# Kernel optimization log

Measured on AMD Instinct MI355X. Metric: run time of the kernel, lower is better.

Reference implementation:

```python
import jax, jax.numpy as jnp
import numpy as np

ALPHA = 0.05   # propalpha
GDEP = 2       # gcn_depth
DIL = 2        # new_dilation
KSET = (2, 3, 6, 7)

def _dconv(x, w, b, d):
    # Conv2d(c_in, c_out, (1, k), dilation=(1, d), padding='same'), NCHW layout
    k = w.shape[-1]
    tot = d * (k - 1)
    lo = tot // 2
    y = jax.lax.conv_general_dilated(x, w, (1, 1), ((0, 0), (lo, tot - lo)),
                                     rhs_dilation=(1, d),
                                     dimension_numbers=('NCHW', 'OIHW', 'NCHW'))
    return y + b[None, :, None, None]

def _inception(x, ws, bs):
    # 'same' padding keeps seq_len for every branch, so the tail-slice is a no-op
    return jnp.concatenate([_dconv(x, w, b, DIL) for w, b in zip(ws, bs)], axis=1)

def _gcn(Hf, Aoff, W, b, n):
    # PyG GCNConv with unit edge weights (no edge_weight passed) and remaining self-loops:
    # out = D^-1/2 (A_off + I_R)^T D^-1/2 (Hf @ W^T) + b, where only rows < n carry edges.
    XW = Hf @ W.T
    deg = jnp.ones((Hf.shape[0],), Hf.dtype).at[:n].add(jnp.sum(Aoff, axis=0))
    dis = jax.lax.rsqrt(deg)
    out = XW / deg[:, None]                                           # self-loop term
    out = out.at[:n].add(dis[:n, None] * (Aoff.T @ (dis[:n, None] * XW[:n])))
    return out + b[None, :]

def _mixprop(X, A, gws, gbs, mw, mb):
    B, C, n, L = X.shape
    # dense_to_sparse ignores weights here (none passed to GCNConv) -> binary adjacency;
    # add_remaining_self_loops replaces any diagonal entries, so zero the diagonal.
    Aoff = (A != 0).astype(X.dtype) * (1.0 - jnp.eye(n, dtype=X.dtype))
    H = X
    hops = [X]
    for i in range(GDEP):
        Hf = H.reshape(B * L, C * n)   # torch row-major reshape, replicated exactly
        H1 = _gcn(Hf, Aoff, gws[i], gbs[i], n)
        H = ALPHA * X + H1.reshape(B, C, n, L)
        hops.append(H)
    Hc = jnp.concatenate(hops, axis=1)  # (B, (GDEP+1)*C, n, L)
    return jnp.einsum('bixl,oi->boxl', Hc, mw) + mb[None, :, None, None]

def _layernorm(x, w, b, idx, eps=1e-5):
    # F.layer_norm over all of x.shape[1:] with node-indexed affine params
    mu = jnp.mean(x, axis=(1, 2, 3), keepdims=True)
    var = jnp.var(x, axis=(1, 2, 3), keepdims=True)
    xh = (x - mu) * jax.lax.rsqrt(var + eps)
    return xh * w[:, idx, :][None] + b[:, idx, :][None]

def _forward(x, x_skip, A, idx, fws, fbs, gws, gbs, skip_w, skip_b,
             mp1_gw, mp1_gb, mp1_mw, mp1_mb, mp2_gw, mp2_gb, mp2_mw, mp2_mb,
             ln_w, ln_b):
    x_res = x
    xf = jnp.tanh(_inception(x, fws, fbs))
    xg = jax.nn.sigmoid(_inception(x, gws, gbs))
    x = xf * xg  # gated dilated temporal conv (dropout is an eval-mode no-op)
    x_skip = jnp.einsum('bixl,oi->boxl', x, skip_w) + skip_b[None, :, None, None] + x_skip
    x = (_mixprop(x, A, mp1_gw, mp1_gb, mp1_mw, mp1_mb)
         + _mixprop(x.swapaxes(0, 0), A.T, mp2_gw, mp2_gb, mp2_mw, mp2_mb))
    x = x + x_res[..., -x.shape[3]:]
    x = _layernorm(x, ln_w, ln_b, idx)
    return x, x_skip

def setup_inputs():
    key = jax.random.key(0)
    ks = jax.random.split(key, 32)
    B, C, N, L, SKIP = 16, 32, 128, 128, 64
    F = C * N
    co = C // len(KSET)
    d = {}
    d['x'] = jax.random.normal(ks[0], (B, C, N, L), jnp.float32)
    d['x_skip'] = jax.random.normal(ks[1], (B, SKIP, N, L), jnp.float32)
    d['A'] = jax.random.uniform(ks[2], (N, N), jnp.float32)
    d['idx'] = jnp.arange(N, dtype=jnp.int32)
    i = 3
    for pre in ('f', 'g'):
        for k in KSET:
            d[pre + 'w' + str(k)] = jax.random.normal(ks[i], (co, C, 1, k), jnp.float32) * float(1.0 / np.sqrt(C * k))
            d[pre + 'b' + str(k)] = jax.random.uniform(ks[i + 1], (co,), jnp.float32)
            i += 2
    d['skip_w'] = jax.random.normal(ks[i], (SKIP, C), jnp.float32) * float(1.0 / np.sqrt(C)); i += 1
    d['skip_b'] = jax.random.uniform(ks[i], (SKIP,), jnp.float32); i += 1
    for mp in ('mp1', 'mp2'):
        d[mp + '_gw'] = jax.random.normal(ks[i], (GDEP, F, F), jnp.float32) * float(1.0 / np.sqrt(F)); i += 1
        d[mp + '_gb'] = jnp.zeros((GDEP, F), jnp.float32)
        d[mp + '_mw'] = jax.random.normal(ks[i], (C, (GDEP + 1) * C), jnp.float32) * float(1.0 / np.sqrt((GDEP + 1) * C)); i += 1
        d[mp + '_mb'] = jax.random.uniform(ks[i], (C,), jnp.float32); i += 1
    d['ln_w'] = jnp.ones((C, N, L), jnp.float32)
    d['ln_b'] = jnp.zeros((C, N, L), jnp.float32)
    return d

def reference(x, x_skip, A, idx, fw2, fb2, fw3, fb3, fw6, fb6, fw7, fb7,
              gw2, gb2, gw3, gb3, gw6, gb6, gw7, gb7, skip_w, skip_b,
              mp1_gw, mp1_gb, mp1_mw, mp1_mb, mp2_gw, mp2_gb, mp2_mw, mp2_mb,
              ln_w, ln_b):
    return _forward(x, x_skip, A, idx,
                    [fw2, fw3, fw6, fw7], [fb2, fb3, fb6, fb7],
                    [gw2, gw3, gw6, gw7], [gb2, gb3, gb6, gb7],
                    skip_w, skip_b, mp1_gw, mp1_gb, mp1_mw, mp1_mb,
                    mp2_gw, mp2_gb, mp2_mw, mp2_mb, ln_w, ln_b)
```

## Files before the change

### kernel.cpp

```cpp
#include <hip/hip_runtime.h>
#include <stdint.h>

typedef unsigned short u16;
typedef unsigned int   u32;
typedef __attribute__((ext_vector_type(4))) float f32x4;
typedef __attribute__((ext_vector_type(8))) short bf16x8;

__device__ __forceinline__ u16 f2bf(float f) {
    u32 i = __float_as_uint(f);
    u32 r = (i + 0x7fffu + ((i >> 16) & 1u)) >> 16;
    return (u16)r;
}
__device__ __forceinline__ float bf2f(u16 u) {
    return __uint_as_float(((u32)u) << 16);
}
__device__ __forceinline__ u32 cvt2bf(float a, float b) {
    u32 r;
    asm("v_cvt_pk_bf16_f32 %0, %1, %2" : "=v"(r) : "v"(a), "v"(b));
    return r;
}

#define GLOAD16(g, l) __builtin_amdgcn_global_load_lds( \
    (const __attribute__((address_space(1))) void*)(g), \
    (__attribute__((address_space(3))) void*)(l), 16, 0, 0)

#define RAW_BARRIER()  asm volatile("s_barrier" ::: "memory")
#define VMCNT(n)       asm volatile("s_waitcnt vmcnt(" #n ")" ::: "memory")

__global__ void k_prep(const float* __restrict__ A, float* dis1, float* inv1,
                       float* dis2, float* inv2)
{
    int r = threadIdx.x;
    if (r >= 128) return;
    int cc = 0, cr = 0;
    for (int j = 0; j < 128; ++j) {
        if (j == r) continue;
        if (A[(j << 7) + r] != 0.f) cc++;
        if (A[(r << 7) + j] != 0.f) cr++;
    }
    float d1 = 1.f + (float)cc, d2 = 1.f + (float)cr;
    dis1[r] = rsqrtf(d1); inv1[r] = 1.f / d1;
    dis2[r] = rsqrtf(d2); inv2[r] = 1.f / d2;
}

__global__ __launch_bounds__(256)
void k_wcvt2(const float* __restrict__ W0, const float* __restrict__ W1,
             u16* __restrict__ Wb0, u16* __restrict__ Wb1)
{
    int half = blockIdx.x >> 13;
    const float* W = half ? W1 : W0;
    u16* Wb = half ? Wb1 : Wb0;
    size_t e = ((size_t)(blockIdx.x & 8191) * 256 + threadIdx.x) * 8;
    f32x4 a = *(const f32x4*)(W + e);
    f32x4 b = *(const f32x4*)(W + e + 4);
    uint4 r;
    r.x = cvt2bf(a[0], a[1]); r.y = cvt2bf(a[2], a[3]);
    r.z = cvt2bf(b[0], b[1]); r.w = cvt2bf(b[2], b[3]);
    *(uint4*)(Wb + e) = r;
}

__global__ __launch_bounds__(512, 1)
void k_gemm2g(const u16* __restrict__ A0, const u16* __restrict__ A1,
              const u16* __restrict__ B0, const u16* __restrict__ B1,
              const u16* __restrict__ Gres,
              const float* __restrict__ gb0, const float* __restrict__ gb1,
              u16* __restrict__ Ha, u16* __restrict__ Hb,
              float* __restrict__ XW0a, float* __restrict__ XW0b)
{
    __shared__ alignas(16) u16 LDS[65536];
    const int NT = 128;
    const int tid  = threadIdx.x;
    const int lane = tid & 63;
    const int wid  = tid >> 6;
    const int wr = wid >> 2, wc = wid & 3;

    const int bid = blockIdx.x;
    const int swz = (bid & 7) * 32 + (bid >> 3);
    const int z   = swz >> 7;
    const int rem = swz & 127;
    const int bm = (rem >> 4) * 256;
    const int bn = (rem & 15) * 256;

    const u16* Ap = (z ? A1 : A0) + (size_t)bm * 4096;
    const u16* Bp = (z ? B1 : B0) + (size_t)bn * 4096;

    int aoff[8], boff[4];
    #pragma unroll
    for (int i = 0; i < 8; ++i) {
        int row = wr * 128 + i * 16 + (lane & 15);
        int sp  = (lane >> 4) ^ ((row >> 1) & 3);
        aoff[i] = row * 32 + sp * 8;
    }
    #pragma unroll
    for (int j = 0; j < 4; ++j) {
        int row = wc * 64 + j * 16 + (lane & 15);
        int sp  = (lane >> 4) ^ ((row >> 1) & 3);
        boff[j] = row * 32 + sp * 8;
    }

    auto stage = [&](int t) {
        const int k0  = t << 5;
        u16* buf = LDS + ((t & 3) << 14);
        #pragma unroll
        for (int h = 0; h < 2; ++h) {
            const int c  = tid + h * 512;
            const int r  = c >> 2;
            const int sl = (c & 3) ^ ((r >> 1) & 3);
            GLOAD16(Ap + (size_t)r * 4096 + k0 + sl * 8, buf + c * 8);
            GLOAD16(Bp + (size_t)r * 4096 + k0 + sl * 8, buf + 8192 + c * 8);
        }
    };

    f32x4 acc[8][4] = {};

    auto compute = [&](int t) {
        const u16* buf = LDS + ((t & 3) << 14);
        bf16x8 af[8], bf[4];
        #pragma unroll
        for (int j = 0; j < 4; ++j) bf[j] = *(const bf16x8*)(buf + 8192 + boff[j]);
        #pragma unroll
        for (int i = 0; i < 8; ++i) af[i] = *(const bf16x8*)(buf + aoff[i]);
        __builtin_amdgcn_s_setprio(1);
        #pragma unroll
        for (int i = 0; i < 8; ++i)
            #pragma unroll
            for (int j = 0; j < 4; ++j)
                acc[i][j] = __builtin_amdgcn_mfma_f32_16x16x32_bf16(af[i], bf[j], acc[i][j], 0, 0, 0);
        __builtin_amdgcn_s_setprio(0);
    };

    stage(0); stage(1); stage(2);
    for (int t = 0; t < NT - 3; ++t) {
        VMCNT(8);
        RAW_BARRIER();
        stage(t + 3);
        compute(t);
    }
    VMCNT(8);  RAW_BARRIER(); compute(NT - 3);
    VMCNT(4);  RAW_BARRIER(); compute(NT - 2);
    VMCNT(0);  RAW_BARRIER(); compute(NT - 1);

    const int orow = (lane >> 4) * 4, ocol = lane & 15;
    const float* gbv = z ? gb1 : gb0;
    u16* H = z ? Hb : Ha;

    #pragma unroll
    for (int j = 0; j < 4; ++j) {
        const int o = bn + wc * 64 + j * 16 + ocol;
        const float gbo = gbv[o];
        #pragma unroll
        for (int i = 0; i < 8; ++i) {
            const int rbase = bm + wr * 128 + i * 16 + orow;
            #pragma unroll
            for (int v = 0; v < 4; ++v) {
                const size_t e = (size_t)(rbase + v) * 4096 + o;
                float g = bf2f(Gres[e]);
                H[e] = f2bf(__fmaf_rn(0.05f, g, acc[i][j][v] + gbo));
            }
        }
    }
    if (bm == 0 && wr == 0) {
        float* XW0 = z ? XW0b : XW0a;
        #pragma unroll
        for (int i = 0; i < 8; ++i) {
            #pragma unroll
            for (int j = 0; j < 4; ++j) {
                float* cp = XW0 + (size_t)(i * 16 + orow) * 4096 + (bn + wc * 64 + j * 16 + ocol);
                #pragma unroll
                for (int v = 0; v < 4; ++v)
                    cp[(size_t)v * 4096] = acc[i][j][v];
            }
        }
    }
}

__global__ __launch_bounds__(256)
void k_gcnfix(const float* __restrict__ XW0a, const float* __restrict__ XW0b,
              const u16* __restrict__ G, const float* __restrict__ Af,
              const float* __restrict__ dis1, const float* __restrict__ inv1,
              const float* __restrict__ dis2, const float* __restrict__ inv2,
              const float* __restrict__ gb0, const float* __restrict__ gb1,
              u16* __restrict__ Ha, u16* __restrict__ Hb)
{
    const int prob = blockIdx.x >> 9;
    const int rem  = blockIdx.x & 511;
    const int t4 = rem * 256 + threadIdx.x;
    const int r = t4 >> 10, og = (t4 & 1023) << 2;
    const float* XW0 = prob ? XW0b : XW0a;
    const float* dis = prob ? dis2 : dis1;
    const float* inv = prob ? inv2 : inv1;
    const float* gb  = prob ? gb1  : gb0;
    u16* H = prob ? Hb : Ha;

    const size_t e = ((size_t)r << 12) + og;
    f32x4 xw = *(const f32x4*)(XW0 + e);
    f32x4 s = {0.f, 0.f, 0.f, 0.f};
    for (int j = 0; j < 128; ++j) {
        float av = prob ? Af[(r << 7) + j] : Af[(j << 7) + r];
        float wv = ((av != 0.f) && (j != r)) ? dis[j] : 0.f;
        f32x4 xv = *(const f32x4*)(XW0 + ((size_t)j << 12) + og);
        #pragma unroll
        for (int q = 0; q < 4; ++q) s[q] = __fmaf_rn(wv, xv[q], s[q]);
    }
    const float iv = inv[r], dr = dis[r];
    f32x4 gb4 = *(const f32x4*)(gb + og);
    uint2 gv = *(const uint2*)(G + e);
    float g0 = __uint_as_float(gv.x << 16), g1 = __uint_as_float(gv.x & 0xffff0000u);
    float g2 = __uint_as_float(gv.y << 16), g3 = __uint_as_float(gv.y & 0xffff0000u);
    float y0 = __fmaf_rn(0.05f, g0, __fmaf_rn(dr, s[0], xw[0] * iv) + gb4[0]);
    float y1 = __fmaf_rn(0.05f, g1, __fmaf_rn(dr, s[1], xw[1] * iv) + gb4[1]);
    float y2 = __fmaf_rn(0.05f, g2, __fmaf_rn(dr, s[2], xw[2] * iv) + gb4[2]);
    float y3 = __fmaf_rn(0.05f, g3, __fmaf_rn(dr, s[3], xw[3] * iv) + gb4[3]);
    uint2 rr;
    rr.x = cvt2bf(y0, y1);
    rr.y = cvt2bf(y2, y3);
    *(uint2*)(H + e) = rr;
}

__device__ __forceinline__ constexpr int wbase_of(int k) {
    return k == 2 ? 0 : k == 3 ? 520 : k == 6 ? 1296 : 2840;
}
__device__ __forceinline__ constexpr int ob_of(int k) {
    return k == 2 ? 0 : k == 3 ? 8 : k == 6 ? 16 : 24;
}

template<int K_>
__device__ __forceinline__ void conv_phase(const float* __restrict__ xsb,
                                           const float* __restrict__ wfp,
                                           const float* __restrict__ wgp,
                                           float fb, float gb,
                                           u16* __restrict__ Gp)
{
    float accf[8], accg[8];
    #pragma unroll
    for (int i = 0; i < 8; ++i) { accf[i] = fb; accg[i] = gb; }
    for (int c = 0; c < 32; ++c) {
        float xw[24];
        const float* xr = xsb + c * 144;
        #pragma unroll
        for (int q = 0; q < 6; ++q) {
            f32x4 v = *(const f32x4*)(xr + q * 4);
            xw[q * 4 + 0] = v[0]; xw[q * 4 + 1] = v[1];
            xw[q * 4 + 2] = v[2]; xw[q * 4 + 3] = v[3];
        }
        float wfj[K_], wgj[K_];
        const float* wfc = wfp + c * K_;
        const float* wgc = wgp + c * K_;
        #pragma unroll
        for (int j = 0; j < K_; ++j) { wfj[j] = wfc[j]; wgj[j] = wgc[j]; }
        #pragma unroll
        for (int li = 0; li < 8; ++li) {
            #pragma unroll
            for (int j = 0; j < K_; ++j) {
                float xv = xw[li + 8 - (K_ - 1) + 2 * j];
                accf[li] = __fmaf_rn(xv, wfj[j], accf[li]);
                accg[li] = __fmaf_rn(xv, wgj[j], accg[li]);
            }
        }
    }
    u16 o8[8];
    #pragma unroll
    for (int i = 0; i < 8; ++i) {
        float e2 = __expf(2.f * accf[i]);
        float th = 1.f - __fdividef(2.f, e2 + 1.f);
        float sg = __fdividef(1.f, 1.f + __expf(-accg[i]));
        o8[i] = f2bf(th * sg);
    }
    uint4 u;
    u.x = o8[0] | ((u32)o8[1] << 16); u.y = o8[2] | ((u32)o8[3] << 16);
    u.z = o8[4] | ((u32)o8[5] << 16); u.w = o8[6] | ((u32)o8[7] << 16);
    *(uint4*)Gp = u;
}

template<int KA, int KB>
__device__ __forceinline__ void wave_pair(const float* __restrict__ xs,
                                          const float* __restrict__ wfl,
                                          const float* __restrict__ wgl,
                                          const float* __restrict__ fbl,
                                          const float* __restrict__ gbl,
                                          int oo, int lL, int b, int n,
                                          u16* __restrict__ G)
{
    {
        constexpr int BS = wbase_of(KA), ST = 32 * KA + 1, OB = ob_of(KA);
        const int o = OB + oo, l0 = lL * 8;
        conv_phase<KA>(xs + l0, wfl + BS + oo * ST, wgl + BS + oo * ST,
                       fbl[o], gbl[o],
                       G + (((size_t)(b * 32 + o) * 128 + n) * 128 + l0));
    }
    {
        constexpr int BS = wbase_of(KB), ST = 32 * KB + 1, OB = ob_of(KB);
        const int o = OB + oo, l0 = 64 + lL * 8;
        conv_phase<KB>(xs + l0, wfl + BS + oo * ST, wgl + BS + oo * ST,
                       fbl[o], gbl[o],
                       G + (((size_t)(b * 32 + o) * 128 + n) * 128 + l0));
    }
}

__global__ __launch_bounds__(256)
void k_incep(const float* __restrict__ x,
             const float* __restrict__ fw2p, const float* __restrict__ fw3p,
             const float* __restrict__ fw6p, const float* __restrict__ fw7p,
             const float* __restrict__ fb2p, const float* __restrict__ fb3p,
             const float* __restrict__ fb6p, const float* __restrict__ fb7p,
             const float* __restrict__ gw2p, const float* __restrict__ gw3p,
             const float* __restrict__ gw6p, const float* __restrict__ gw7p,
             const float* __restrict__ gb2p, const float* __restrict__ gb3p,
             const float* __restrict__ gb6p, const float* __restrict__ gb7p,
             u16* __restrict__ G)
{
    __shared__ alignas(16) float xs[32 * 144];
    __shared__ float wfl[4640], wgl[4640];
    __shared__ float fbl[32], gbl[32];
    const int tid = threadIdx.x;
    const int b = blockIdx.x >> 7, n = blockIdx.x & 127;

    for (int i = tid; i < 32 * 144; i += 256) xs[i] = 0.f;
    for (int g = tid; g < 4608; g += 256) {
        int rel, k, woff;
        const float *pf, *pg;
        if (g < 512)       { rel = g;        k = 2; woff = 0;    pf = fw2p; pg = gw2p; }
        else if (g < 1280) { rel = g - 512;  k = 3; woff = 520;  pf = fw3p; pg = gw3p; }
        else if (g < 2816) { rel = g - 1280; k = 6; woff = 1296; pf = fw6p; pg = gw6p; }
        else               { rel = g - 2816; k = 7; woff = 2840; pf = fw7p; pg = gw7p; }
        int ck = 32 * k;
        int oo = rel / ck, rem = rel % ck;
        int dst = woff + oo * (ck + 1) + rem;
        wfl[dst] = pf[rel];
        wgl[dst] = pg[rel];
    }
    if (tid < 32) {
        int br = tid >> 3, oo = tid & 7;
        const float* pf = br == 0 ? fb2p : br == 1 ? fb3p : br == 2 ? fb6p : fb7p;
        const float* pg = br == 0 ? gb2p : br == 1 ? gb3p : br == 2 ? gb6p : gb7p;
        fbl[tid] = pf[oo]; gbl[tid] = pg[oo];
    }
    __syncthreads();
    const float* xb = x + (size_t)b * 524288 + n * 128;
    for (int p = 0; p < 4; ++p) {
        int chunk = p * 256 + tid;
        int c = chunk >> 5, l4 = (chunk & 31) * 4;
        *(f32x4*)&xs[c * 144 + 8 + l4] = *(const f32x4*)(xb + (size_t)c * 16384 + l4);
    }
    __syncthreads();

    const int w = tid >> 6, lane = tid & 63;
    const int oo = lane >> 3, lL = lane & 7;
    switch (w) {
        case 0:  wave_pair<2, 7>(xs, wfl, wgl, fbl, gbl, oo, lL, b, n, G); break;
        case 1:  wave_pair<7, 2>(xs, wfl, wgl, fbl, gbl, oo, lL, b, n, G); break;
        case 2:  wave_pair<3, 6>(xs, wfl, wgl, fbl, gbl, oo, lL, b, n, G); break;
        default: wave_pair<6, 3>(xs, wfl, wgl, fbl, gbl, oo, lL, b, n, G); break;
    }
}

__global__ __launch_bounds__(256)
void k_skip(const u16* __restrict__ G, const float* __restrict__ xskip,
            const float* __restrict__ sw, const float* __restrict__ sb,
            float* __restrict__ outp)
{
    __shared__ alignas(16) u16 Gs[4096];
    __shared__ float swl[64 * 33];
    __shared__ float sbl[64];
    const int tid = threadIdx.x;
    const int b = blockIdx.x >> 7, n = blockIdx.x & 127;
    const u16* gb_ = G + (size_t)b * 524288 + n * 128;
    for (int p = 0; p < 2; ++p) {
        int chunk = p * 256 + tid, c = chunk >> 4, l8 = (chunk & 15) * 8;
        *(uint4*)&Gs[c * 128 + l8] = *(const uint4*)(gb_ + (size_t)c * 16384 + l8);
    }
    for (int i = tid; i < 2048; i += 256) swl[(i >> 5) * 33 + (i & 31)] = sw[i];
    if (tid < 64) sbl[tid] = sb[tid];
    __syncthreads();
    const int sg = (tid & 15) * 4, l0 = (tid >> 4) * 8;
    float acc[4][8];
    #pragma unroll
    for (int si = 0; si < 4; ++si) {
        float bv = sbl[sg + si];
        #pragma unroll
        for (int li = 0; li < 8; ++li) acc[si][li] = bv;
    }
    for (int c = 0; c < 32; ++c) {
        uint4 gv = *(const uint4*)&Gs[c * 128 + l0];
        float g[8];
        g[0] = __uint_as_float(gv.x << 16); g[1] = __uint_as_float(gv.x & 0xffff0000u);
        g[2] = __uint_as_float(gv.y << 16); g[3] = __uint_as_float(gv.y & 0xffff0000u);
        g[4] = __uint_as_float(gv.z << 16); g[5] = __uint_as_float(gv.z & 0xffff0000u);
        g[6] = __uint_as_float(gv.w << 16); g[7] = __uint_as_float(gv.w & 0xffff0000u);
        #pragma unroll
        for (int si = 0; si < 4; ++si) {
            float wv = swl[(sg + si) * 33 + c];
            #pragma unroll
            for (int li = 0; li < 8; ++li) acc[si][li] = __fmaf_rn(g[li], wv, acc[si][li]);
        }
    }
    #pragma unroll
    for (int si = 0; si < 4; ++si) {
        size_t e = ((size_t)(b * 64 + sg + si) * 128 + n) * 128 + l0;
        f32x4 x0 = *(const f32x4*)(xskip + e);
        f32x4 x1 = *(const f32x4*)(xskip + e + 4);
        f32x4 r0, r1;
        r0[0] = acc[si][0] + x0[0]; r0[1] = acc[si][1] + x0[1];
        r0[2] = acc[si][2] + x0[2]; r0[3] = acc[si][3] + x0[3];
        r1[0] = acc[si][4] + x1[0]; r1[1] = acc[si][5] + x1[1];
        r1[2] = acc[si][6] + x1[2]; r1[3] = acc[si][7] + x1[3];
        *(f32x4*)(outp + e)     = r0;
        *(f32x4*)(outp + e + 4) = r1;
    }
}

__global__ __launch_bounds__(256)
void k_mix2ln(const u16* __restrict__ G,
              const u16* __restrict__ H1, const u16* __restrict__ H2,
              const u16* __restrict__ H1b, const u16* __restrict__ H2b,
              const float* __restrict__ mw1, const float* __restrict__ mb1,
              const float* __restrict__ mw2, const float* __restrict__ mb2,
              const float* __restrict__ x,
              float* __restrict__ Y, float* __restrict__ partial)
{
    __shared__ alignas(16) u16 Gs[4096], H1s[4096], H2s[4096], H1bs[4096], H2bs[4096];
    __shared__ float wSg[32 * 33], wS11[32 * 33], wS12[32 * 33], wS21[32 * 33], wS22[32 * 33];
    __shared__ float mbl[32];
    const int tid = threadIdx.x;
    const int b = blockIdx.x >> 7, xn = blockIdx.x & 127;
    size_t base = (size_t)b * 524288 + xn * 128;
    for (int p = 0; p < 2; ++p) {
        int chunk = p * 256 + tid, c = chunk >> 4, l8 = (chunk & 15) * 8;
        size_t src = base + (size_t)c * 16384 + l8;
        *(uint4*)&Gs[c * 128 + l8]   = *(const uint4*)(G + src);
        *(uint4*)&H1s[c * 128 + l8]  = *(const uint4*)(H1 + src);
        *(uint4*)&H2s[c * 128 + l8]  = *(const uint4*)(H2 + src);
        *(uint4*)&H1bs[c * 128 + l8] = *(const uint4*)(H1b + src);
        *(uint4*)&H2bs[c * 128 + l8] = *(const uint4*)(H2b + src);
    }
    for (int i = tid; i < 1024; i += 256) {
        int o = i >> 5, c = i & 31;
        int d = o * 33 + c;
        wSg[d]  = mw1[o * 96 + c] + mw2[o * 96 + c];
        wS11[d] = mw1[o * 96 + 32 + c];
        wS12[d] = mw1[o * 96 + 64 + c];
        wS21[d] = mw2[o * 96 + 32 + c];
        wS22[d] = mw2[o * 96 + 64 + c];
    }
    if (tid < 32) mbl[tid] = mb1[tid] + mb2[tid];
    __syncthreads();
    const int og = (tid & 7) * 4, l0 = (tid >> 3) * 4;
    float acc[4][4];
    #pragma unroll
    for (int oi = 0; oi < 4; ++oi) {
        float bv = mbl[og + oi];
        acc[oi][0] = bv; acc[oi][1] = bv; acc[oi][2] = bv; acc[oi][3] = bv;
    }
    for (int c = 0; c < 32; ++c) {
        uint2 ga = *(const uint2*)&Gs[c * 128 + l0];
        uint2 h1 = *(const uint2*)&H1s[c * 128 + l0];
        uint2 h2 = *(const uint2*)&H2s[c * 128 + l0];
        uint2 j1 = *(const uint2*)&H1bs[c * 128 + l0];
        uint2 j2 = *(const uint2*)&H2bs[c * 128 + l0];
        float gv[4], v1[4], v2[4], u1[4], u2[4];
        gv[0] = __uint_as_float(ga.x << 16); gv[1] = __uint_as_float(ga.x & 0xffff0000u);
        gv[2] = __uint_as_float(ga.y << 16); gv[3] = __uint_as_float(ga.y & 0xffff0000u);
        v1[0] = __uint_as_float(h1.x << 16); v1[1] = __uint_as_float(h1.x & 0xffff0000u);
        v1[2] = __uint_as_float(h1.y << 16); v1[3] = __uint_as_float(h1.y & 0xffff0000u);
        v2[0] = __uint_as_float(h2.x << 16); v2[1] = __uint_as_float(h2.x & 0xffff0000u);
        v2[2] = __uint_as_float(h2.y << 16); v2[3] = __uint_as_float(h2.y & 0xffff0000u);
        u1[0] = __uint_as_float(j1.x << 16); u1[1] = __uint_as_float(j1.x & 0xffff0000u);
        u1[2] = __uint_as_float(j1.y << 16); u1[3] = __uint_as_float(j1.y & 0xffff0000u);
        u2[0] = __uint_as_float(j2.x << 16); u2[1] = __uint_as_float(j2.x & 0xffff0000u);
        u2[2] = __uint_as_float(j2.y << 16); u2[3] = __uint_as_float(j2.y & 0xffff0000u);
        #pragma unroll
        for (int oi = 0; oi < 4; ++oi) {
            int d = (og + oi) * 33 + c;
            float a0 = wSg[d], a1 = wS11[d], a2 = wS12[d], a3 = wS21[d], a4 = wS22[d];
            #pragma unroll
            for (int li = 0; li < 4; ++li)
                acc[oi][li] += gv[li] * a0 + v1[li] * a1 + v2[li] * a2
                             + u1[li] * a3 + u2[li] * a4;
        }
    }
    float s = 0.f, ss = 0.f;
    #pragma unroll
    for (int oi = 0; oi < 4; ++oi) {
        size_t e = ((size_t)(b * 32 + og + oi) * 128 + xn) * 128 + l0;
        f32x4 xv = *(const f32x4*)(x + e);
        f32x4 yv;
        #pragma unroll
        for (int li = 0; li < 4; ++li) {
            float y = acc[oi][li] + xv[li];
            yv[li] = y;
            s += y; ss += y * y;
        }
        *(f32x4*)(Y + e) = yv;
    }
    #pragma unroll
    for (int o = 32; o > 0; o >>= 1) {
        s  += __shfl_down(s,  o, 64);
        ss += __shfl_down(ss, o, 64);
    }
    __shared__ float sred[8];
    int w = tid >> 6;
    if ((tid & 63) == 0) { sred[w * 2] = s; sred[w * 2 + 1] = ss; }
    __syncthreads();
    if (tid == 0) {
        partial[blockIdx.x * 2]     = sred[0] + sred[2] + sred[4] + sred[6];
        partial[blockIdx.x * 2 + 1] = sred[1] + sred[3] + sred[5] + sred[7];
    }
}

__global__ __launch_bounds__(256)
void k_lnnorm(const float* __restrict__ Y,
              const float* __restrict__ partial, const int* __restrict__ idxp,
              const float* __restrict__ lnw, const float* __restrict__ lnb,
              float* __restrict__ outx)
{
    const int tid = threadIdx.x;
    const int b = blockIdx.x >> 7, chunk = blockIdx.x & 127;
    float s = 0.f, ss = 0.f;
    if (tid < 128) {
        s  = partial[(b * 128 + tid) * 2];
        ss = partial[(b * 128 + tid) * 2 + 1];
    }
    #pragma unroll
    for (int o = 32; o > 0; o >>= 1) {
        s  += __shfl_down(s,  o, 64);
        ss += __shfl_down(ss, o, 64);
    }
    __shared__ float sred[4];
    __shared__ float mv[2];
    if ((tid & 63) == 0 && tid < 128) { sred[(tid >> 6) * 2] = s; sred[(tid >> 6) * 2 + 1] = ss; }
    __syncthreads();
    if (tid == 0) {
        float S = sred[0] + sred[2], SS = sred[1] + sred[3];
        float mean = S * (1.f / 524288.f);
        float var = SS * (1.f / 524288.f) - mean * mean;
        mv[0] = mean; mv[1] = rsqrtf(var + 1e-5f);
    }
    __syncthreads();
    const float mean = mv[0], rstd = mv[1];
    #pragma unroll
    for (int q = 0; q < 4; ++q) {
        int ib = chunk * 4096 + q * 1024 + tid * 4;
        size_t e = (size_t)b * 524288 + ib;
        f32x4 yv = *(const f32x4*)(Y + e);
        int c = ib >> 14, xn = (ib >> 7) & 127, l = ib & 127;
        int ix = idxp[xn];
        size_t we = ((size_t)c * 128 + ix) * 128 + l;
        f32x4 wv = *(const f32x4*)(lnw + we);
        f32x4 bv = *(const f32x4*)(lnb + we);
        f32x4 r;
        #pragma unroll
        for (int j = 0; j < 4; ++j)
            r[j] = (yv[j] - mean) * rstd * wv[j] + bv[j];
        *(f32x4*)(outx + e) = r;
    }
}

extern "C" void kernel_launch(void* const* d_in, const int* in_sizes, int n_in,
                              void* d_out, int out_size, void* d_ws, size_t ws_size,
                              hipStream_t stream)
{
    (void)in_sizes; (void)n_in; (void)out_size; (void)ws_size;
    const float* x      = (const float*)d_in[0];
    const float* xskip  = (const float*)d_in[1];
    const float* A      = (const float*)d_in[2];
    const int*   idxp   = (const int*)d_in[3];
    const float* fw2p = (const float*)d_in[4];  const float* fb2p = (const float*)d_in[5];
    const float* fw3p = (const float*)d_in[6];  const float* fb3p = (const float*)d_in[7];
    const float* fw6p = (const float*)d_in[8];  const float* fb6p = (const float*)d_in[9];
    const float* fw7p = (const float*)d_in[10]; const float* fb7p = (const float*)d_in[11];
    const float* gw2p = (const float*)d_in[12]; const float* gb2p = (const float*)d_in[13];
    const float* gw3p = (const float*)d_in[14]; const float* gb3p = (const float*)d_in[15];
    const float* gw6p = (const float*)d_in[16]; const float* gb6p = (const float*)d_in[17];
    const float* gw7p = (const float*)d_in[18]; const float* gb7p = (const float*)d_in[19];
    const float* sw   = (const float*)d_in[20]; const float* sb   = (const float*)d_in[21];
    const float* mp1_gw = (const float*)d_in[22]; const float* mp1_gb = (const float*)d_in[23];
    const float* mp1_mw = (const float*)d_in[24]; const float* mp1_mb = (const float*)d_in[25];
    const float* mp2_gw = (const float*)d_in[26]; const float* mp2_gb = (const float*)d_in[27];
    const float* mp2_mw = (const float*)d_in[28]; const float* mp2_mb = (const float*)d_in[29];
    const float* lnw = (const float*)d_in[30]; const float* lnb = (const float*)d_in[31];

    char* wsb = (char*)d_ws;
    float* out_x  = (float*)d_out;
    float* out_sk = out_x + 8388608;

    const size_t MB16 = 16777216, MB33 = 33554432;
    u16*   G    = (u16*)(wsb);
    u16*   H1   = (u16*)(wsb + MB16);
    u16*   H1b  = (u16*)(wsb + 2 * MB16);
    u16*   H2   = (u16*)(wsb + 3 * MB16);
    u16*   H2b  = (u16*)(wsb + 4 * MB16);
    u16*   Wb0  = (u16*)(wsb + 5 * MB16);
    u16*   Wb1  = (u16*)(wsb + 5 * MB16 + MB33);
    float* Yb   = (float*)Wb0;
    float* XW0a = (float*)(wsb + 5 * MB16 + 2 * MB33);
    float* XW0b = (float*)(wsb + 5 * MB16 + 2 * MB33 + 2097152);
    float* part = (float*)(wsb + 5 * MB16 + 2 * MB33 + 4194304);
    float* dd   = (float*)(wsb + 5 * MB16 + 2 * MB33 + 4194304 + 16384);
    float *dis1 = dd, *inv1 = dd + 128, *dis2 = dd + 256, *inv2 = dd + 384;

    k_prep<<<1, 128, 0, stream>>>(A, dis1, inv1, dis2, inv2);
    k_incep<<<2048, 256, 0, stream>>>(x, fw2p, fw3p, fw6p, fw7p, fb2p, fb3p, fb6p, fb7p,
                                      gw2p, gw3p, gw6p, gw7p, gb2p, gb3p, gb6p, gb7p, G);
    k_skip<<<2048, 256, 0, stream>>>(G, xskip, sw, sb, out_sk);

    k_wcvt2<<<16384, 256, 0, stream>>>(mp1_gw, mp2_gw, Wb0, Wb1);
    k_gemm2g<<<256, 512, 0, stream>>>(G, G, Wb0, Wb1, G, mp1_gb, mp2_gb,
                                      H1, H1b, XW0a, XW0b);
    k_gcnfix<<<1024, 256, 0, stream>>>(XW0a, XW0b, G, A, dis1, inv1, dis2, inv2,
                                       mp1_gb, mp2_gb, H1, H1b);
    k_wcvt2<<<16384, 256, 0, stream>>>(mp1_gw + MB16, mp2_gw + MB16, Wb0, Wb1);
    k_gemm2g<<<256, 512, 0, stream>>>(H1, H1b, Wb0, Wb1, G, mp1_gb + 4096, mp2_gb + 4096,
                                      H2, H2b, XW0a, XW0b);
    k_gcnfix<<<1024, 256, 0, stream>>>(XW0a, XW0b, G, A, dis1, inv1, dis2, inv2,
                                       mp1_gb + 4096, mp2_gb + 4096, H2, H2b);
    k_mix2ln<<<2048, 256, 0, stream>>>(G, H1, H2, H1b, H2b, mp1_mw, mp1_mb,
                                       mp2_mw, mp2_mb, x, Yb, part);
    k_lnnorm<<<2048, 256, 0, stream>>>(Yb, part, idxp, lnw, lnb, out_x);
}
```

Measured before the change: 672.7 us.

## Double-buffer LDS fragment reads in registers to overlap with MFMA

```diff
diff --git a/kernel.cpp b/kernel.cpp
--- a/kernel.cpp
+++ b/kernel.cpp
@@ -99,6 +99,7 @@
     }
 
     auto stage = [&](int t) {
+        if (t >= NT) return;
         const int k0  = t << 5;
         u16* buf = LDS + ((t & 3) << 14);
         #pragma unroll
@@ -112,33 +113,49 @@
     };
 
     f32x4 acc[8][4] = {};
-
-    auto compute = [&](int t) {
+    bf16x8 fA0[8], fB0[4], fA1[8], fB1[4];
+
+    auto readFrags = [&](int t, bf16x8* fa, bf16x8* fb) {
         const u16* buf = LDS + ((t & 3) << 14);
-        bf16x8 af[8], bf[4];
-        #pragma unroll
-        for (int j = 0; j < 4; ++j) bf[j] = *(const bf16x8*)(buf + 8192 + boff[j]);
-        #pragma unroll
-        for (int i = 0; i < 8; ++i) af[i] = *(const bf16x8*)(buf + aoff[i]);
+        #pragma unroll
+        for (int j = 0; j < 4; ++j) fb[j] = *(const bf16x8*)(buf + 8192 + boff[j]);
+        #pragma unroll
+        for (int i = 0; i < 8; ++i) fa[i] = *(const bf16x8*)(buf + aoff[i]);
+    };
+    auto mfmaAll = [&](const bf16x8* fa, const bf16x8* fb) {
         __builtin_amdgcn_s_setprio(1);
         #pragma unroll
         for (int i = 0; i < 8; ++i)
             #pragma unroll
             for (int j = 0; j < 4; ++j)
-                acc[i][j] = __builtin_amdgcn_mfma_f32_16x16x32_bf16(af[i], bf[j], acc[i][j], 0, 0, 0);
+                acc[i][j] = __builtin_amdgcn_mfma_f32_16x16x32_bf16(fa[i], fb[j], acc[i][j], 0, 0, 0);
         __builtin_amdgcn_s_setprio(0);
     };
 
-    stage(0); stage(1); stage(2);
-    for (int t = 0; t < NT - 3; ++t) {
-        VMCNT(8);
+    stage(0); stage(1);
+    VMCNT(4);
+    RAW_BARRIER();
+    readFrags(0, fA0, fB0);
+    stage(2);
+
+    for (int i = 0; i < 63; ++i) {
+        const int t = 2 * i;
+        VMCNT(4);
         RAW_BARRIER();
         stage(t + 3);
-        compute(t);
-    }
-    VMCNT(8);  RAW_BARRIER(); compute(NT - 3);
-    VMCNT(4);  RAW_BARRIER(); compute(NT - 2);
-    VMCNT(0);  RAW_BARRIER(); compute(NT - 1);
+        readFrags(t + 1, fA1, fB1);
+        mfmaAll(fA0, fB0);
+        VMCNT(4);
+        RAW_BARRIER();
+        stage(t + 4);
+        readFrags(t + 2, fA0, fB0);
+        mfmaAll(fA1, fB1);
+    }
+    VMCNT(0);
+    RAW_BARRIER();
+    readFrags(127, fA1, fB1);
+    mfmaAll(fA0, fB0);
+    mfmaAll(fA1, fB1);
 
     const int orow = (lane >> 4) * 4, ocol = lane & 15;
     const float* gbv = z ? gb1 : gb0;
```

Result: no change. 682.5 us (+1.5%).

## Shrink GEMM tiles to 128x256 with 4 waves, triple-buffered; store LN input as bf16

Applied to the files above, without the earlier changes.

```diff
diff --git a/kernel.cpp b/kernel.cpp
--- a/kernel.cpp
+++ b/kernel.cpp
@@ -59,7 +59,7 @@
     *(uint4*)(Wb + e) = r;
 }
 
-__global__ __launch_bounds__(512, 1)
+__global__ __launch_bounds__(256, 2)
 void k_gemm2g(const u16* __restrict__ A0, const u16* __restrict__ A1,
               const u16* __restrict__ B0, const u16* __restrict__ B1,
               const u16* __restrict__ Gres,
@@ -67,18 +67,17 @@
               u16* __restrict__ Ha, u16* __restrict__ Hb,
               float* __restrict__ XW0a, float* __restrict__ XW0b)
 {
-    __shared__ alignas(16) u16 LDS[65536];
+    __shared__ alignas(16) u16 LDS[36864];
     const int NT = 128;
     const int tid  = threadIdx.x;
     const int lane = tid & 63;
-    const int wid  = tid >> 6;
-    const int wr = wid >> 2, wc = wid & 3;
+    const int wc   = tid >> 6;
 
     const int bid = blockIdx.x;
-    const int swz = (bid & 7) * 32 + (bid >> 3);
-    const int z   = swz >> 7;
-    const int rem = swz & 127;
-    const int bm = (rem >> 4) * 256;
+    const int swz = (bid & 7) * 64 + (bid >> 3);
+    const int z   = swz >> 8;
+    const int rem = swz & 255;
+    const int bm = (rem >> 4) * 128;
     const int bn = (rem & 15) * 256;
 
     const u16* Ap = (z ? A1 : A0) + (size_t)bm * 4096;
@@ -87,7 +86,7 @@
     int aoff[8], boff[4];
     #pragma unroll
     for (int i = 0; i < 8; ++i) {
-        int row = wr * 128 + i * 16 + (lane & 15);
+        int row = i * 16 + (lane & 15);
         int sp  = (lane >> 4) ^ ((row >> 1) & 3);
         aoff[i] = row * 32 + sp * 8;
     }
@@ -95,29 +94,35 @@
     for (int j = 0; j < 4; ++j) {
         int row = wc * 64 + j * 16 + (lane & 15);
         int sp  = (lane >> 4) ^ ((row >> 1) & 3);
-        boff[j] = row * 32 + sp * 8;
+        boff[j] = 4096 + row * 32 + sp * 8;
     }
 
     auto stage = [&](int t) {
-        const int k0  = t << 5;
-        u16* buf = LDS + ((t & 3) << 14);
+        const int k0 = t << 5;
+        u16* buf = LDS + (t % 3) * 12288;
         #pragma unroll
         for (int h = 0; h < 2; ++h) {
-            const int c  = tid + h * 512;
+            const int c  = tid + h * 256;
             const int r  = c >> 2;
             const int sl = (c & 3) ^ ((r >> 1) & 3);
             GLOAD16(Ap + (size_t)r * 4096 + k0 + sl * 8, buf + c * 8);
-            GLOAD16(Bp + (size_t)r * 4096 + k0 + sl * 8, buf + 8192 + c * 8);
+        }
+        #pragma unroll
+        for (int h = 0; h < 4; ++h) {
+            const int c  = tid + h * 256;
+            const int r  = c >> 2;
+            const int sl = (c & 3) ^ ((r >> 1) & 3);
+            GLOAD16(Bp + (size_t)r * 4096 + k0 + sl * 8, buf + 4096 + c * 8);
         }
     };
 
     f32x4 acc[8][4] = {};
 
     auto compute = [&](int t) {
-        const u16* buf = LDS + ((t & 3) << 14);
+        const u16* buf = LDS + (t % 3) * 12288;
         bf16x8 af[8], bf[4];
         #pragma unroll
-        for (int j = 0; j < 4; ++j) bf[j] = *(const bf16x8*)(buf + 8192 + boff[j]);
+        for (int j = 0; j < 4; ++j) bf[j] = *(const bf16x8*)(buf + boff[j]);
         #pragma unroll
         for (int i = 0; i < 8; ++i) af[i] = *(const bf16x8*)(buf + aoff[i]);
         __builtin_amdgcn_s_setprio(1);
@@ -129,16 +134,17 @@
         __builtin_amdgcn_s_setprio(0);
     };
 
-    stage(0); stage(1); stage(2);
-    for (int t = 0; t < NT - 3; ++t) {
-        VMCNT(8);
+    stage(0); stage(1);
+    for (int t = 0; t < NT - 2; ++t) {
+        VMCNT(6);
         RAW_BARRIER();
-        stage(t + 3);
+        stage(t + 2);
         compute(t);
     }
-    VMCNT(8);  RAW_BARRIER(); compute(NT - 3);
-    VMCNT(4);  RAW_BARRIER(); compute(NT - 2);
-    VMCNT(0);  RAW_BARRIER(); compute(NT - 1);
+    VMCNT(0);
+    RAW_BARRIER();
+    compute(NT - 2);
+    compute(NT - 1);
 
     const int orow = (lane >> 4) * 4, ocol = lane & 15;
     const float* gbv = z ? gb1 : gb0;
@@ -150,7 +156,7 @@
         const float gbo = gbv[o];
         #pragma unroll
         for (int i = 0; i < 8; ++i) {
-            const int rbase = bm + wr * 128 + i * 16 + orow;
+            const int rbase = bm + i * 16 + orow;
             #pragma unroll
             for (int v = 0; v < 4; ++v) {
                 const size_t e = (size_t)(rbase + v) * 4096 + o;
@@ -159,7 +165,7 @@
             }
         }
     }
-    if (bm == 0 && wr == 0) {
+    if (bm == 0) {
         float* XW0 = z ? XW0b : XW0a;
         #pragma unroll
         for (int i = 0; i < 8; ++i) {
@@ -416,7 +422,7 @@
               const float* __restrict__ mw1, const float* __restrict__ mb1,
               const float* __restrict__ mw2, const float* __restrict__ mb2,
               const float* __restrict__ x,
-              float* __restrict__ Y, float* __restrict__ partial)
+              u16* __restrict__ Y, float* __restrict__ partial)
 {
     __shared__ alignas(16) u16 Gs[4096], H1s[4096], H2s[4096], H1bs[4096], H2bs[4096];
     __shared__ float wSg[32 * 33], wS11[32 * 33], wS12[32 * 33], wS21[32 * 33], wS22[32 * 33];
@@ -483,14 +489,16 @@
     for (int oi = 0; oi < 4; ++oi) {
         size_t e = ((size_t)(b * 32 + og + oi) * 128 + xn) * 128 + l0;
         f32x4 xv = *(const f32x4*)(x + e);
-        f32x4 yv;
-        #pragma unroll
-        for (int li = 0; li < 4; ++li) {
-            float y = acc[oi][li] + xv[li];
-            yv[li] = y;
-            s += y; ss += y * y;
-        }
-        *(f32x4*)(Y + e) = yv;
+        float y0 = acc[oi][0] + xv[0];
+        float y1 = acc[oi][1] + xv[1];
+        float y2 = acc[oi][2] + xv[2];
+        float y3 = acc[oi][3] + xv[3];
+        s  += y0 + y1 + y2 + y3;
+        ss += y0 * y0 + y1 * y1 + y2 * y2 + y3 * y3;
+        uint2 rr;
+        rr.x = cvt2bf(y0, y1);
+        rr.y = cvt2bf(y2, y3);
+        *(uint2*)(Y + e) = rr;
     }
     #pragma unroll
     for (int o = 32; o > 0; o >>= 1) {
@@ -508,7 +516,7 @@
 }
 
 __global__ __launch_bounds__(256)
-void k_lnnorm(const float* __restrict__ Y,
+void k_lnnorm(const u16* __restrict__ Y,
               const float* __restrict__ partial, const int* __restrict__ idxp,
               const float* __restrict__ lnw, const float* __restrict__ lnb,
               float* __restrict__ outx)
@@ -541,7 +549,10 @@
     for (int q = 0; q < 4; ++q) {
         int ib = chunk * 4096 + q * 1024 + tid * 4;
         size_t e = (size_t)b * 524288 + ib;
-        f32x4 yv = *(const f32x4*)(Y + e);
+        uint2 yv2 = *(const uint2*)(Y + e);
+        float y[4];
+        y[0] = __uint_as_float(yv2.x << 16); y[1] = __uint_as_float(yv2.x & 0xffff0000u);
+        y[2] = __uint_as_float(yv2.y << 16); y[3] = __uint_as_float(yv2.y & 0xffff0000u);
         int c = ib >> 14, xn = (ib >> 7) & 127, l = ib & 127;
         int ix = idxp[xn];
         size_t we = ((size_t)c * 128 + ix) * 128 + l;
@@ -550,7 +561,7 @@
         f32x4 r;
         #pragma unroll
         for (int j = 0; j < 4; ++j)
-            r[j] = (yv[j] - mean) * rstd * wv[j] + bv[j];
+            r[j] = (y[j] - mean) * rstd * wv[j] + bv[j];
         *(f32x4*)(outx + e) = r;
     }
 }
@@ -591,7 +602,7 @@
     u16*   H2b  = (u16*)(wsb + 4 * MB16);
     u16*   Wb0  = (u16*)(wsb + 5 * MB16);
     u16*   Wb1  = (u16*)(wsb + 5 * MB16 + MB33);
-    float* Yb   = (float*)Wb0;
+    u16*   Yb   = (u16*)Wb0;
     float* XW0a = (float*)(wsb + 5 * MB16 + 2 * MB33);
     float* XW0b = (float*)(wsb + 5 * MB16 + 2 * MB33 + 2097152);
     float* part = (float*)(wsb + 5 * MB16 + 2 * MB33 + 4194304);
@@ -604,12 +615,12 @@
     k_skip<<<2048, 256, 0, stream>>>(G, xskip, sw, sb, out_sk);
 
     k_wcvt2<<<16384, 256, 0, stream>>>(mp1_gw, mp2_gw, Wb0, Wb1);
-    k_gemm2g<<<256, 512, 0, stream>>>(G, G, Wb0, Wb1, G, mp1_gb, mp2_gb,
+    k_gemm2g<<<512, 256, 0, stream>>>(G, G, Wb0, Wb1, G, mp1_gb, mp2_gb,
                                       H1, H1b, XW0a, XW0b);
     k_gcnfix<<<1024, 256, 0, stream>>>(XW0a, XW0b, G, A, dis1, inv1, dis2, inv2,
                                        mp1_gb, mp2_gb, H1, H1b);
     k_wcvt2<<<16384, 256, 0, stream>>>(mp1_gw + MB16, mp2_gw + MB16, Wb0, Wb1);
-    k_gemm2g<<<256, 512, 0, stream>>>(H1, H1b, Wb0, Wb1, G, mp1_gb + 4096, mp2_gb + 4096,
+    k_gemm2g<<<512, 256, 0, stream>>>(H1, H1b, Wb0, Wb1, G, mp1_gb + 4096, mp2_gb + 4096,
                                       H2, H2b, XW0a, XW0b);
     k_gcnfix<<<1024, 256, 0, stream>>>(XW0a, XW0b, G, A, dis1, inv1, dis2, inv2,
                                        mp1_gb + 4096, mp2_gb + 4096, H2, H2b);
```

Result: slower. 696.6 us (+3.6%).
